# Kernel optimization log

Hardware: AMD Instinct MI355X
Metric: run time of the kernel (lower is better)

Reference implementation:

```python
import jax, jax.numpy as jnp
import numpy as np

BATCH, SEQ, DIM = 4, 4096, 2048
NUM_EXPERTS, TOP_K, RANK = 8, 2, 16
SCALING = 1.0


def setup_inputs() -> dict:
    key = jax.random.key(0)
    k0, k1, k2, k3 = jax.random.split(key, 4)
    s = 0.02
    x = jax.random.normal(k0, (BATCH, SEQ, DIM), dtype=jnp.float32)
    gate_W = jax.random.normal(k1, (NUM_EXPERTS, DIM), dtype=jnp.float32) * s  # [E, D] torch Linear layout
    gate_b = jnp.zeros((NUM_EXPERTS,), dtype=jnp.float32)
    A = jax.random.normal(k2, (NUM_EXPERTS, RANK, DIM), dtype=jnp.float32) * s   # lora_A weights [E, R, D]
    Bm = jax.random.normal(k3, (NUM_EXPERTS, DIM, RANK), dtype=jnp.float32) * s  # lora_B weights [E, D, R]
    return {"x": x, "gate_W": gate_W, "gate_b": gate_b, "A": A, "Bm": Bm}


def reference(x, gate_W, gate_b, A, Bm):
    # Gate: logits [B, S, E], softmax probs
    logits = jnp.einsum('bsd,ed->bse', x, gate_W) + gate_b
    gate_probs = jax.nn.softmax(logits, axis=-1)
    # Top-k selection. NOTE: the original torch code computes topk weights but
    # NEVER uses them -- expert outputs are summed unweighted over the top-k set.
    _, idx = jax.lax.top_k(gate_probs, TOP_K)  # idx: [B, S, K]
    # mask[b,s,e] = expert e is in token (b,s)'s top-k
    mask = jnp.any(idx[..., :, None] == jnp.arange(NUM_EXPERTS), axis=-2)  # [B, S, E] bool
    # Dense grouped LoRA: h [B, S, E, R] (small, rank=16), masked before combine
    h = jnp.einsum('bsd,erd->bser', x, A)
    h = jax.nn.gelu(h, approximate=False) * mask[..., None].astype(x.dtype)
    out = jnp.einsum('bser,edr->bsd', h, Bm) * SCALING  # [B, S, D]
    return out, gate_probs
```

## Files before the change

### kernel.cpp

```cpp
#include <hip/hip_runtime.h>
#include <math.h>

#define NTOK 16384
#define DIM  2048
#define NEXP 8
#define RANK 16

typedef unsigned short ushort_t;
typedef unsigned int   uint_t;
typedef __attribute__((ext_vector_type(8))) short bf16x8;
typedef __attribute__((ext_vector_type(4))) float f32x4;

__device__ __forceinline__ ushort_t f2bf(float f) {
  union { float f; uint_t u; } v; v.f = f;
  uint_t r = (v.u + 0x7FFFu + ((v.u >> 16) & 1u)) >> 16;
  return (ushort_t)r;
}
__device__ __forceinline__ float bf2f(ushort_t s) {
  union { uint_t u; float f; } v; v.u = ((uint_t)s) << 16;
  return v.f;
}

__device__ __forceinline__ void gl_lds16(const ushort_t* g, ushort_t* l) {
  __builtin_amdgcn_global_load_lds(
      (const __attribute__((address_space(1))) unsigned int*)g,
      (__attribute__((address_space(3))) unsigned int*)l, 16, 0, 0);
}

__global__ __launch_bounds__(256) void k0_prep(
    const float* __restrict__ gW, const float* __restrict__ A,
    const float* __restrict__ Bm,
    ushort_t* __restrict__ Wc, ushort_t* __restrict__ Bm2) {
  int b = blockIdx.x, t = threadIdx.x;
  if (b < 1280) {
    int idx = b * 256 + t;
    int r = idx >> 11, d = idx & 2047;
    float v;
    if (r < 8)        v = gW[r * 2048 + d];
    else if (r < 16)  v = 0.f;
    else if (r < 144) v = A[(size_t)(r - 16) * 2048 + d];
    else if (r < 152) { float g = gW[(r - 144) * 2048 + d]; v = g - bf2f(f2bf(g)); }
    else              v = 0.f;
    int ch = d >> 6, c = d & 63;
    int cs = ((((c >> 3) ^ (r & 7)) << 3) | (c & 7));
    Wc[((size_t)ch * 160 + r) * 64 + cs] = f2bf(v);
  } else {
    int idx = (b - 1280) * 256 + t;
    int dd = idx >> 7, c = idx & 127, e = c >> 4, rr = c & 15;
    Bm2[idx] = f2bf(Bm[((size_t)e * 2048 + dd) * 16 + rr]);
  }
}

#define BKP 72

__global__ __launch_bounds__(512) void k1_fused(
    const float* __restrict__ x, const float* __restrict__ gate_b,
    const ushort_t* __restrict__ Wc, const ushort_t* __restrict__ Bm2,
    float* __restrict__ out, float* __restrict__ probs) {
  __shared__ __align__(16) ushort_t ws_w[2][160 * 64];
  __shared__ __align__(16) ushort_t xs_hi[2][32][BKP];
  __shared__ __align__(16) ushort_t xs_lo[2][32][BKP];
  __shared__ float Cs[32][152];
  __shared__ int sel0s[32], sel1s[32];
  ushort_t* hm_s = &ws_w[0][0];

  const int t = threadIdx.x;
  const int lane = t & 63, wave = t >> 6;
  const int l15 = lane & 15, q = lane >> 4;
  const int mt = wave & 1;
  const int ng = wave >> 1;
  const int tile0 = (ng == 3) ? 6 : ng * 2;
  const int ntiles = (ng == 3) ? 3 : 2;
  const int tok0 = blockIdx.x * 32;

  f32x4 acc[3];
  #pragma unroll
  for (int i = 0; i < 3; ++i) acc[i] = (f32x4)0.f;

  const float4* xg = (const float4*)(x + (size_t)tok0 * DIM);
  const int xrow = t >> 4, xc4 = t & 15;

  float4 xv;

  auto load_x = [&](int ch) {
    xv = xg[xrow * (DIM / 4) + ch * 16 + xc4];
  };
  auto stage_w = [&](int ch, int buf) {
    const ushort_t* src = Wc + (size_t)ch * (160 * 64);
    for (int i = wave; i < 20; i += 8)
      gl_lds16(src + (size_t)(i * 64 + lane) * 8, &ws_w[buf][i * 512]);
  };
  auto write_x = [&](int buf) {
    float vv[4] = {xv.x, xv.y, xv.z, xv.w};
    ushort_t h4[4], l4[4];
    #pragma unroll
    for (int j = 0; j < 4; ++j) {
      h4[j] = f2bf(vv[j]);
      l4[j] = f2bf(vv[j] - bf2f(h4[j]));
    }
    *(uint2*)&xs_hi[buf][xrow][xc4 * 4] = *(const uint2*)h4;
    *(uint2*)&xs_lo[buf][xrow][xc4 * 4] = *(const uint2*)l4;
  };

  load_x(0);
  stage_w(0, 0);
  write_x(0);
  __syncthreads();

  for (int ch = 0; ch < 32; ++ch) {
    const int cur = ch & 1, nxt = cur ^ 1;
    if (ch < 31) { load_x(ch + 1); stage_w(ch + 1, nxt); }

    const ushort_t* wb = ws_w[cur];
    auto wfrag = [&](int r, int kkg) -> bf16x8 {
      int pos = (r << 3) + ((kkg + q) ^ (r & 7));
      return *(const bf16x8*)&wb[pos << 3];
    };

    #pragma unroll
    for (int kk = 0; kk < 64; kk += 32) {
      const int kkg = kk >> 3;
      bf16x8 ah = *(const bf16x8*)&xs_hi[cur][mt * 16 + l15][kk + q * 8];
      if (ng == 0) {
        bf16x8 al  = *(const bf16x8*)&xs_lo[cur][mt * 16 + l15][kk + q * 8];
        bf16x8 bgl = wfrag(144 + l15, kkg);
        bf16x8 b0  = wfrag(l15, kkg);
        acc[0] = __builtin_amdgcn_mfma_f32_16x16x32_bf16(ah, b0, acc[0], 0, 0, 0);
        acc[0] = __builtin_amdgcn_mfma_f32_16x16x32_bf16(al, b0, acc[0], 0, 0, 0);
        acc[0] = __builtin_amdgcn_mfma_f32_16x16x32_bf16(ah, bgl, acc[0], 0, 0, 0);
        bf16x8 b1 = wfrag(16 + l15, kkg);
        acc[1] = __builtin_amdgcn_mfma_f32_16x16x32_bf16(ah, b1, acc[1], 0, 0, 0);
      } else {
        #pragma unroll
        for (int i = 0; i < 3; ++i) {
          if (i < ntiles) {
            bf16x8 b = wfrag((tile0 + i) * 16 + l15, kkg);
            acc[i] = __builtin_amdgcn_mfma_f32_16x16x32_bf16(ah, b, acc[i], 0, 0, 0);
          }
        }
      }
    }

    if (ch < 31) write_x(nxt);
    __syncthreads();
  }

  #pragma unroll
  for (int i = 0; i < 3; ++i) {
    if (i < ntiles) {
      #pragma unroll
      for (int r = 0; r < 4; ++r)
        Cs[mt * 16 + q * 4 + r][(tile0 + i) * 16 + l15] = acc[i][r];
    }
  }
  __syncthreads();

  if (t < 32) {
    int m = t;
    float lg[NEXP];
    #pragma unroll
    for (int e = 0; e < NEXP; ++e) lg[e] = Cs[m][e] + gate_b[e];
    float mx = lg[0];
    #pragma unroll
    for (int e = 1; e < NEXP; ++e) mx = fmaxf(mx, lg[e]);
    float ex[NEXP], s = 0.f;
    #pragma unroll
    for (int e = 0; e < NEXP; ++e) { ex[e] = __expf(lg[e] - mx); s += ex[e]; }
    float inv = 1.f / s;
    float4 p0 = make_float4(ex[0] * inv, ex[1] * inv, ex[2] * inv, ex[3] * inv);
    float4 p1 = make_float4(ex[4] * inv, ex[5] * inv, ex[6] * inv, ex[7] * inv);
    float* pp = probs + (size_t)(tok0 + m) * NEXP;
    *(float4*)pp = p0; *(float4*)(pp + 4) = p1;
    int i0 = 0;
    #pragma unroll
    for (int e = 1; e < NEXP; ++e) if (lg[e] > lg[i0]) i0 = e;
    int i1 = (i0 == 0) ? 1 : 0;
    #pragma unroll
    for (int e = 0; e < NEXP; ++e) if (e != i0 && lg[e] > lg[i1]) i1 = e;
    sel0s[m] = i0; sel1s[m] = i1;
  }
  __syncthreads();

  if (t < 256) {
    int m = t >> 3, e = t & 7;
    int on = (e == sel0s[m]) | (e == sel1s[m]);
    ushort_t ov[16];
    #pragma unroll
    for (int r = 0; r < RANK; ++r) {
      float v = Cs[m][16 + e * 16 + r];
      float g = on ? (0.5f * v * (1.f + erff(v * 0.70710678118654752f))) : 0.f;
      ov[r] = f2bf(g);
    }
    int g0 = (2 * e) ^ (m & 7), g1 = (2 * e + 1) ^ (m & 7);
    *(uint4*)&hm_s[m * 128 + g0 * 8] = *(const uint4*)&ov[0];
    *(uint4*)&hm_s[m * 128 + g1 * 8] = *(const uint4*)&ov[8];
  }
  __syncthreads();

  {
    bf16x8 af[2][4];
    #pragma unroll
    for (int m2 = 0; m2 < 2; ++m2) {
      int tok = m2 * 16 + l15;
      #pragma unroll
      for (int kk = 0; kk < 4; ++kk)
        af[m2][kk] = *(const bf16x8*)&hm_s[tok * 128 + (((kk * 4 + q) ^ (tok & 7)) << 3)];
    }

    const int ncol0 = wave * 256;
    const ushort_t* bp = Bm2 + (size_t)(ncol0 + l15) * 128 + q * 8;

    auto loadB = [&](bf16x8* dst, int i) {
      #pragma unroll
      for (int k = 0; k < 4; ++k)
        dst[k] = *(const bf16x8*)(bp + (size_t)i * 2048 + k * 32);
    };
    auto comp = [&](const bf16x8* bb, int i) {
      #pragma unroll
      for (int m2 = 0; m2 < 2; ++m2) {
        f32x4 c = (f32x4)0.f;
        #pragma unroll
        for (int k = 0; k < 4; ++k)
          c = __builtin_amdgcn_mfma_f32_16x16x32_bf16(bb[k], af[m2][k], c, 0, 0, 0);
        *(f32x4*)&out[(size_t)(tok0 + m2 * 16 + l15) * DIM + ncol0 + i * 16 + q * 4] = c;
      }
    };

    bf16x8 bA[4], bB[4];
    loadB(bA, 0);
    #pragma unroll
    for (int ii = 0; ii < 8; ++ii) {
      loadB(bB, 2 * ii + 1);
      comp(bA, 2 * ii);
      if (ii < 7) loadB(bA, 2 * ii + 2);
      comp(bB, 2 * ii + 1);
    }
  }
}

extern "C" void kernel_launch(void* const* d_in, const int* in_sizes, int n_in,
                              void* d_out, int out_size, void* d_ws, size_t ws_size,
                              hipStream_t stream) {
  const float* x      = (const float*)d_in[0];
  const float* gate_W = (const float*)d_in[1];
  const float* gate_b = (const float*)d_in[2];
  const float* A      = (const float*)d_in[3];
  const float* Bm     = (const float*)d_in[4];

  float* out   = (float*)d_out;
  float* probs = out + (size_t)NTOK * DIM;

  ushort_t* Wc  = (ushort_t*)d_ws;
  ushort_t* Bm2 = Wc + 32 * 160 * 64;

  k0_prep<<<dim3(2304), dim3(256), 0, stream>>>(gate_W, A, Bm, Wc, Bm2);
  k1_fused<<<dim3(NTOK / 32), dim3(512), 0, stream>>>(x, gate_b, Wc, Bm2, out, probs);
}
```

Before: 277.7 us.

## Drop LDS staging in gate/LoRA-A GEMM, load fragments directly from global

Replaces the LDS double-buffered staging of x and the swizzled weight chunks with direct per-lane global loads of x (converted to bf16 hi/lo in registers) and of a plain row-major bf16 weight matrix. This removes the per-chunk __syncthreads and the LDS writes and reads, and shrinks shared memory so that more blocks can be resident (launch bounds now request 4). The cost is that each wave reloads x and weights from L2/global without sharing through LDS, and there is no explicit prefetch across k-chunks, so latency hiding depends on occupancy.

Result: slower. 363.9 us (+31.0%).

```diff
diff --git a/kernel.cpp b/kernel.cpp
--- a/kernel.cpp
+++ b/kernel.cpp
@@ -21,16 +21,29 @@
   return v.f;
 }
 
-__device__ __forceinline__ void gl_lds16(const ushort_t* g, ushort_t* l) {
-  __builtin_amdgcn_global_load_lds(
-      (const __attribute__((address_space(1))) unsigned int*)g,
-      (__attribute__((address_space(3))) unsigned int*)l, 16, 0, 0);
+__device__ __forceinline__ bf16x8 cvt_hi(float4 a, float4 b) {
+  ushort_t h[8];
+  h[0] = f2bf(a.x); h[1] = f2bf(a.y); h[2] = f2bf(a.z); h[3] = f2bf(a.w);
+  h[4] = f2bf(b.x); h[5] = f2bf(b.y); h[6] = f2bf(b.z); h[7] = f2bf(b.w);
+  return *(const bf16x8*)h;
+}
+__device__ __forceinline__ bf16x8 cvt_lo(float4 a, float4 b, bf16x8 hi) {
+  ushort_t l[8];
+  l[0] = f2bf(a.x - bf2f((ushort_t)hi[0]));
+  l[1] = f2bf(a.y - bf2f((ushort_t)hi[1]));
+  l[2] = f2bf(a.z - bf2f((ushort_t)hi[2]));
+  l[3] = f2bf(a.w - bf2f((ushort_t)hi[3]));
+  l[4] = f2bf(b.x - bf2f((ushort_t)hi[4]));
+  l[5] = f2bf(b.y - bf2f((ushort_t)hi[5]));
+  l[6] = f2bf(b.z - bf2f((ushort_t)hi[6]));
+  l[7] = f2bf(b.w - bf2f((ushort_t)hi[7]));
+  return *(const bf16x8*)l;
 }
 
 __global__ __launch_bounds__(256) void k0_prep(
     const float* __restrict__ gW, const float* __restrict__ A,
     const float* __restrict__ Bm,
-    ushort_t* __restrict__ Wc, ushort_t* __restrict__ Bm2) {
+    ushort_t* __restrict__ Wt, ushort_t* __restrict__ Bm2) {
   int b = blockIdx.x, t = threadIdx.x;
   if (b < 1280) {
     int idx = b * 256 + t;
@@ -41,9 +54,7 @@
     else if (r < 144) v = A[(size_t)(r - 16) * 2048 + d];
     else if (r < 152) { float g = gW[(r - 144) * 2048 + d]; v = g - bf2f(f2bf(g)); }
     else              v = 0.f;
-    int ch = d >> 6, c = d & 63;
-    int cs = ((((c >> 3) ^ (r & 7)) << 3) | (c & 7));
-    Wc[((size_t)ch * 160 + r) * 64 + cs] = f2bf(v);
+    Wt[(size_t)r * 2048 + d] = f2bf(v);
   } else {
     int idx = (b - 1280) * 256 + t;
     int dd = idx >> 7, c = idx & 127, e = c >> 4, rr = c & 15;
@@ -51,98 +62,73 @@
   }
 }
 
-#define BKP 72
-
-__global__ __launch_bounds__(512) void k1_fused(
+__global__ __launch_bounds__(512, 4) void k1_fused(
     const float* __restrict__ x, const float* __restrict__ gate_b,
-    const ushort_t* __restrict__ Wc, const ushort_t* __restrict__ Bm2,
+    const ushort_t* __restrict__ Wt, const ushort_t* __restrict__ Bm2,
     float* __restrict__ out, float* __restrict__ probs) {
-  __shared__ __align__(16) ushort_t ws_w[2][160 * 64];
-  __shared__ __align__(16) ushort_t xs_hi[2][32][BKP];
-  __shared__ __align__(16) ushort_t xs_lo[2][32][BKP];
   __shared__ float Cs[32][152];
+  __shared__ __align__(16) ushort_t hm_s[32][128];
   __shared__ int sel0s[32], sel1s[32];
-  ushort_t* hm_s = &ws_w[0][0];
 
   const int t = threadIdx.x;
   const int lane = t & 63, wave = t >> 6;
   const int l15 = lane & 15, q = lane >> 4;
   const int mt = wave & 1;
   const int ng = wave >> 1;
-  const int tile0 = (ng == 3) ? 6 : ng * 2;
   const int ntiles = (ng == 3) ? 3 : 2;
   const int tok0 = blockIdx.x * 32;
+  const int tok  = tok0 + mt * 16 + l15;
+
+  const int rb0 = ng * 32;
+  const ushort_t* w0 = Wt + (size_t)(rb0 + l15) * DIM + q * 8;
+  const ushort_t* w1 = Wt + (size_t)(rb0 + 16 + l15) * DIM + q * 8;
+  const ushort_t* w2 = Wt + (size_t)(((ng == 0) ? 144 : 128) + l15) * DIM + q * 8;
+  const float* xr = x + (size_t)tok * DIM + q * 8;
 
   f32x4 acc[3];
   #pragma unroll
   for (int i = 0; i < 3; ++i) acc[i] = (f32x4)0.f;
 
-  const float4* xg = (const float4*)(x + (size_t)tok0 * DIM);
-  const int xrow = t >> 4, xc4 = t & 15;
-
-  float4 xv;
-
-  auto load_x = [&](int ch) {
-    xv = xg[xrow * (DIM / 4) + ch * 16 + xc4];
-  };
-  auto stage_w = [&](int ch, int buf) {
-    const ushort_t* src = Wc + (size_t)ch * (160 * 64);
-    for (int i = wave; i < 20; i += 8)
-      gl_lds16(src + (size_t)(i * 64 + lane) * 8, &ws_w[buf][i * 512]);
-  };
-  auto write_x = [&](int buf) {
-    float vv[4] = {xv.x, xv.y, xv.z, xv.w};
-    ushort_t h4[4], l4[4];
-    #pragma unroll
-    for (int j = 0; j < 4; ++j) {
-      h4[j] = f2bf(vv[j]);
-      l4[j] = f2bf(vv[j] - bf2f(h4[j]));
-    }
-    *(uint2*)&xs_hi[buf][xrow][xc4 * 4] = *(const uint2*)h4;
-    *(uint2*)&xs_lo[buf][xrow][xc4 * 4] = *(const uint2*)l4;
-  };
-
-  load_x(0);
-  stage_w(0, 0);
-  write_x(0);
-  __syncthreads();
-
   for (int ch = 0; ch < 32; ++ch) {
-    const int cur = ch & 1, nxt = cur ^ 1;
-    if (ch < 31) { load_x(ch + 1); stage_w(ch + 1, nxt); }
-
-    const ushort_t* wb = ws_w[cur];
-    auto wfrag = [&](int r, int kkg) -> bf16x8 {
-      int pos = (r << 3) + ((kkg + q) ^ (r & 7));
-      return *(const bf16x8*)&wb[pos << 3];
-    };
-
-    #pragma unroll
-    for (int kk = 0; kk < 64; kk += 32) {
-      const int kkg = kk >> 3;
-      bf16x8 ah = *(const bf16x8*)&xs_hi[cur][mt * 16 + l15][kk + q * 8];
-      if (ng == 0) {
-        bf16x8 al  = *(const bf16x8*)&xs_lo[cur][mt * 16 + l15][kk + q * 8];
-        bf16x8 bgl = wfrag(144 + l15, kkg);
-        bf16x8 b0  = wfrag(l15, kkg);
-        acc[0] = __builtin_amdgcn_mfma_f32_16x16x32_bf16(ah, b0, acc[0], 0, 0, 0);
-        acc[0] = __builtin_amdgcn_mfma_f32_16x16x32_bf16(al, b0, acc[0], 0, 0, 0);
-        acc[0] = __builtin_amdgcn_mfma_f32_16x16x32_bf16(ah, bgl, acc[0], 0, 0, 0);
-        bf16x8 b1 = wfrag(16 + l15, kkg);
-        acc[1] = __builtin_amdgcn_mfma_f32_16x16x32_bf16(ah, b1, acc[1], 0, 0, 0);
-      } else {
-        #pragma unroll
-        for (int i = 0; i < 3; ++i) {
-          if (i < ntiles) {
-            bf16x8 b = wfrag((tile0 + i) * 16 + l15, kkg);
-            acc[i] = __builtin_amdgcn_mfma_f32_16x16x32_bf16(ah, b, acc[i], 0, 0, 0);
-          }
-        }
-      }
-    }
-
-    if (ch < 31) write_x(nxt);
-    __syncthreads();
+    const int k0c = ch * 64;
+    float4 xa = *(const float4*)(xr + k0c);
+    float4 xb = *(const float4*)(xr + k0c + 4);
+    float4 xc = *(const float4*)(xr + k0c + 32);
+    float4 xd = *(const float4*)(xr + k0c + 36);
+    bf16x8 wA0 = *(const bf16x8*)(w0 + k0c);
+    bf16x8 wA1 = *(const bf16x8*)(w0 + k0c + 32);
+    bf16x8 wB0 = *(const bf16x8*)(w1 + k0c);
+    bf16x8 wB1 = *(const bf16x8*)(w1 + k0c + 32);
+
+    bf16x8 ah0 = cvt_hi(xa, xb), ah1 = cvt_hi(xc, xd);
+
+    if (ng == 0) {
+      bf16x8 wC0 = *(const bf16x8*)(w2 + k0c);
+      bf16x8 wC1 = *(const bf16x8*)(w2 + k0c + 32);
+      bf16x8 al0 = cvt_lo(xa, xb, ah0), al1 = cvt_lo(xc, xd, ah1);
+      acc[0] = __builtin_amdgcn_mfma_f32_16x16x32_bf16(ah0, wA0, acc[0], 0, 0, 0);
+      acc[0] = __builtin_amdgcn_mfma_f32_16x16x32_bf16(al0, wA0, acc[0], 0, 0, 0);
+      acc[0] = __builtin_amdgcn_mfma_f32_16x16x32_bf16(ah0, wC0, acc[0], 0, 0, 0);
+      acc[1] = __builtin_amdgcn_mfma_f32_16x16x32_bf16(ah0, wB0, acc[1], 0, 0, 0);
+      acc[0] = __builtin_amdgcn_mfma_f32_16x16x32_bf16(ah1, wA1, acc[0], 0, 0, 0);
+      acc[0] = __builtin_amdgcn_mfma_f32_16x16x32_bf16(al1, wA1, acc[0], 0, 0, 0);
+      acc[0] = __builtin_amdgcn_mfma_f32_16x16x32_bf16(ah1, wC1, acc[0], 0, 0, 0);
+      acc[1] = __builtin_amdgcn_mfma_f32_16x16x32_bf16(ah1, wB1, acc[1], 0, 0, 0);
+    } else if (ng == 3) {
+      bf16x8 wC0 = *(const bf16x8*)(w2 + k0c);
+      bf16x8 wC1 = *(const bf16x8*)(w2 + k0c + 32);
+      acc[0] = __builtin_amdgcn_mfma_f32_16x16x32_bf16(ah0, wA0, acc[0], 0, 0, 0);
+      acc[1] = __builtin_amdgcn_mfma_f32_16x16x32_bf16(ah0, wB0, acc[1], 0, 0, 0);
+      acc[2] = __builtin_amdgcn_mfma_f32_16x16x32_bf16(ah0, wC0, acc[2], 0, 0, 0);
+      acc[0] = __builtin_amdgcn_mfma_f32_16x16x32_bf16(ah1, wA1, acc[0], 0, 0, 0);
+      acc[1] = __builtin_amdgcn_mfma_f32_16x16x32_bf16(ah1, wB1, acc[1], 0, 0, 0);
+      acc[2] = __builtin_amdgcn_mfma_f32_16x16x32_bf16(ah1, wC1, acc[2], 0, 0, 0);
+    } else {
+      acc[0] = __builtin_amdgcn_mfma_f32_16x16x32_bf16(ah0, wA0, acc[0], 0, 0, 0);
+      acc[1] = __builtin_amdgcn_mfma_f32_16x16x32_bf16(ah0, wB0, acc[1], 0, 0, 0);
+      acc[0] = __builtin_amdgcn_mfma_f32_16x16x32_bf16(ah1, wA1, acc[0], 0, 0, 0);
+      acc[1] = __builtin_amdgcn_mfma_f32_16x16x32_bf16(ah1, wB1, acc[1], 0, 0, 0);
+    }
   }
 
   #pragma unroll
@@ -150,7 +136,7 @@
     if (i < ntiles) {
       #pragma unroll
       for (int r = 0; r < 4; ++r)
-        Cs[mt * 16 + q * 4 + r][(tile0 + i) * 16 + l15] = acc[i][r];
+        Cs[mt * 16 + q * 4 + r][rb0 + i * 16 + l15] = acc[i][r];
     }
   }
   __syncthreads();
@@ -192,8 +178,8 @@
       ov[r] = f2bf(g);
     }
     int g0 = (2 * e) ^ (m & 7), g1 = (2 * e + 1) ^ (m & 7);
-    *(uint4*)&hm_s[m * 128 + g0 * 8] = *(const uint4*)&ov[0];
-    *(uint4*)&hm_s[m * 128 + g1 * 8] = *(const uint4*)&ov[8];
+    *(uint4*)&hm_s[m][g0 * 8] = *(const uint4*)&ov[0];
+    *(uint4*)&hm_s[m][g1 * 8] = *(const uint4*)&ov[8];
   }
   __syncthreads();
 
@@ -201,10 +187,10 @@
     bf16x8 af[2][4];
     #pragma unroll
     for (int m2 = 0; m2 < 2; ++m2) {
-      int tok = m2 * 16 + l15;
+      int tk = m2 * 16 + l15;
       #pragma unroll
       for (int kk = 0; kk < 4; ++kk)
-        af[m2][kk] = *(const bf16x8*)&hm_s[tok * 128 + (((kk * 4 + q) ^ (tok & 7)) << 3)];
+        af[m2][kk] = *(const bf16x8*)&hm_s[tk][(((kk * 4 + q) ^ (tk & 7)) << 3)];
     }
 
     const int ncol0 = wave * 256;
@@ -250,9 +236,9 @@
   float* out   = (float*)d_out;
   float* probs = out + (size_t)NTOK * DIM;
 
-  ushort_t* Wc  = (ushort_t*)d_ws;
-  ushort_t* Bm2 = Wc + 32 * 160 * 64;
-
-  k0_prep<<<dim3(2304), dim3(256), 0, stream>>>(gate_W, A, Bm, Wc, Bm2);
-  k1_fused<<<dim3(NTOK / 32), dim3(512), 0, stream>>>(x, gate_b, Wc, Bm2, out, probs);
-}
+  ushort_t* Wt  = (ushort_t*)d_ws;
+  ushort_t* Bm2 = Wt + 160 * 2048;
+
+  k0_prep<<<dim3(2304), dim3(256), 0, stream>>>(gate_W, A, Bm, Wt, Bm2);
+  k1_fused<<<dim3(NTOK / 32), dim3(512), 0, stream>>>(x, gate_b, Wt, Bm2, out, probs);
+}
```
